# Optimization experiments

Hardware: AMD Instinct MI355X
Metric: run time of the kernel (lower is better)

Reference implementation:

```python
import jax, jax.numpy as jnp
import numpy as np

T, C_IN, H, W = 128, 3, 64, 64
HC = (32, 64)
K = 3


def _conv(x, w, b):
    # x: [1, Cin, H, W], w: [Cout, Cin, K, K] -> SAME padding
    y = jax.lax.conv_general_dilated(
        x, w, window_strides=(1, 1), padding='SAME',
        dimension_numbers=('NCHW', 'OIHW', 'NCHW'))
    return y + b[None, :, None, None]


def _run_layer(xs, w, b, hc):
    # xs: [T, Cin, H, W]; scan the ConvLSTM cell over time (batch = 1)
    h0 = jnp.zeros((1, hc, xs.shape[-2], xs.shape[-1]), xs.dtype)
    c0 = jnp.zeros_like(h0)

    def step(carry, x):
        h, c = carry
        z = _conv(jnp.concatenate([x[None], h], axis=1), w, b)  # [1, 4*hc, H, W]
        i, f, o, g = jnp.split(z, 4, axis=1)
        c_next = jax.nn.sigmoid(f) * c + jax.nn.sigmoid(i) * jnp.tanh(g)
        h_next = jax.nn.sigmoid(o) * jnp.tanh(c_next)
        return (h_next, c_next), h_next[0]

    (h, c), ys = jax.lax.scan(step, (h0, c0), xs)
    return ys, h, c  # ys: [T, hc, H, W]


def setup_inputs() -> dict:
    key = jax.random.key(0)
    ks = jax.random.split(key, 4)
    inp = {
        'input': jax.random.normal(ks[0], (T, C_IN, H, W), jnp.float32),
        'w1': jax.random.normal(ks[1], (4 * HC[0], C_IN + HC[0], K, K), jnp.float32) * 0.05,
        'b1': jnp.zeros((4 * HC[0],), jnp.float32),
        'w2': jax.random.normal(ks[2], (4 * HC[1], HC[0] + HC[1], K, K), jnp.float32) * 0.05,
        'b2': jnp.zeros((4 * HC[1],), jnp.float32),
        'fc_w': jax.random.uniform(ks[3], (6, H * W * HC[1]), jnp.float32, -0.1, 0.1),
        'fc_b': jnp.zeros((6,), jnp.float32),
    }
    return inp


def reference(input, w1, b1, w2, b2, fc_w, fc_b):
    ys1, h1, c1 = _run_layer(input, w1, b1, HC[0])
    ys2, h2, c2 = _run_layer(ys1, w2, b2, HC[1])
    outputs = ys2.reshape(ys2.shape[0], -1)          # [T, hc2*H*W]
    pose_sequence = outputs @ fc_w.T + fc_b          # [T, 6]
    return pose_sequence, h1, c1, h2, c2
```

## Files before the change

### kernel.cpp

```cpp
#include <hip/hip_runtime.h>

typedef _Float16 f16;
typedef _Float16 f16x8 __attribute__((ext_vector_type(8)));
typedef float f32x4 __attribute__((ext_vector_type(4)));
typedef unsigned short ushort_t;
typedef unsigned long long u64_t;


#define IN1SZ 209088
#define IN2ASZ 139392
#define IN2BSZ 278784
#define WP1OFF 1254528
#define WP1SZ 73728
#define WP2OFF (WP1OFF + WP1SZ)
#define WP2SZ 221184
#define FCWPOFF (WP2OFF + WP2SZ)

__device__ __forceinline__ float sigm(float x) {
  return __builtin_amdgcn_rcpf(1.0f + __expf(-x));
}
__device__ __forceinline__ float tanh_fast(float x) {
  float xc = fminf(fmaxf(x, -10.f), 10.f);
  float e = __expf(2.f * xc);
  return (e - 1.f) * __builtin_amdgcn_rcpf(e + 1.f);
}
__device__ __forceinline__ ushort_t f2u(f16 v) { return __builtin_bit_cast(ushort_t, v); }
__device__ __forceinline__ f16x8 u2f(uint4 v) { return __builtin_bit_cast(f16x8, v); }

__global__ __launch_bounds__(256) void pack_kernel(const float* __restrict__ w1,
                                                   const float* __restrict__ w2,
                                                   const float* __restrict__ fcb,
                                                   const float* __restrict__ x0,
                                                   const float* __restrict__ fcw,
                                                   float* __restrict__ pose,
                                                   ushort_t* __restrict__ wp1,
                                                   ushort_t* __restrict__ wp2,
                                                   ushort_t* __restrict__ in1hi0,
                                                   float* __restrict__ fcwp) {
  int i = blockIdx.x * 256 + threadIdx.x;
  if (i < 27648) {
    int lane = i & 63;
    int f = i >> 6;
    int mt = f & 7;
    int sm = f >> 3;
    int s = sm % 27, mb = sm / 27;
    int m = mt * 16 + (lane & 15);
    int rg = mb * 128 + m;
    int h = rg >> 2, G = rg & 3;
    int orow = G * 64 + h;
    int tap = s / 3, cb = (s % 3) * 32;
    int cq = cb + (lane >> 4) * 8;
    for (int j = 0; j < 8; ++j) {
      float v = w2[(orow * 96 + cq + j) * 9 + tap];
      wp2[f * 512 + lane * 8 + j] = f2u((f16)v);
    }
    return;
  }
  i -= 27648;
  if (i < 9216) {
    int lane = i & 63;
    int f = i >> 6;
    int mt = f & 3;
    int sm = f >> 2;
    int s = sm % 18, mb = sm / 18;
    int m = mt * 16 + (lane & 15);
    int rg = mb * 64 + m;
    int h = rg >> 2, G = rg & 3;
    int orow = G * 32 + h;
    int tap = s >> 1, cb = (s & 1) * 32;
    int cq = cb + (lane >> 4) * 8;
    for (int j = 0; j < 8; ++j) {
      int c = cq + j;
      float v = 0.f;
      if (c < 32) v = w1[(orow * 35 + c + 3) * 9 + tap];
      else if (c < 35) v = w1[(orow * 35 + c - 32) * 9 + tap];
      wp1[f * 512 + lane * 8 + j] = f2u((f16)v);
    }
    return;
  }
  i -= 9216;
  if (i < 768) { pose[i] = fcb[i % 6]; return; }
  i -= 768;
  if (i < 12288) {
    int c = i >> 12, pix = i & 4095;
    int y = pix >> 6, x = pix & 63;
    int pidx = ((y + 1) * 66 + (x + 1)) * 48 + 32 + c;
    in1hi0[pidx] = f2u((f16)x0[i]);
    return;
  }
  i -= 12288;
  if (i < 262144) {
    float* dst = fcwp + (size_t)i * 6;
#pragma unroll
    for (int j = 0; j < 6; ++j) dst[j] = fcw[(size_t)j * 262144 + i];
  }
}

template <int LAYER>
__device__ __forceinline__ void conv_body(
    int bid,
    const ushort_t* __restrict__ bhi, const ushort_t* __restrict__ b2hi,
    const ushort_t* __restrict__ wp, const float* __restrict__ bias,
    float* __restrict__ cst, float* __restrict__ hout,
    ushort_t* __restrict__ d1hi,
    ushort_t* __restrict__ d2hi,
    const float* __restrict__ fcwp, float* __restrict__ pose_t,
    const float* __restrict__ xn,
    ushort_t* Bh, ushort_t* hs, float (*red)[6]) {
  constexpr int CS = (LAYER == 1) ? 72 : 104;
  constexpr int NC32 = (LAYER == 1) ? 2 : 3;
  constexpr int NS = 9 * NC32;
  constexpr int MT = (LAYER == 1) ? 4 : 8;
  constexpr int MTPW = (LAYER == 1) ? 1 : 2;
  constexpr int H = (LAYER == 1) ? 32 : 64;
  constexpr int DEPTH = 8;
  constexpr int PRE = DEPTH - 1;

  const int tid = threadIdx.x;
  const int lane = tid & 63;
  const int w = tid >> 6;
  const int mb = bid & 1;
  const int ntile = bid >> 1;
  const int Y0 = (ntile >> 3) * 4;
  const int X0 = (ntile & 7) * 8;

  if (LAYER == 2) {
    for (int i = tid; i < 720; i += 256) {
      int hy = i / 120, rem = i % 120;
      int hx = rem / 12, c8 = rem % 12;
      int pos = (Y0 + hy) * 66 + X0 + hx;
      int dst = (hy * 10 + hx) * CS + c8 * 8;
      if (c8 < 4) {
        *(uint4*)(&Bh[dst]) = *(const uint4*)(&bhi[pos * 32 + c8 * 8]);
      } else {
        *(uint4*)(&Bh[dst]) = *(const uint4*)(&b2hi[pos * 64 + (c8 - 4) * 8]);
      }
    }
  } else {
    for (int i = tid; i < 360; i += 256) {
      int hy = i / 60, rem = i % 60;
      int hx = rem / 6, c8 = (rem % 6) * 8;
      int src = ((Y0 + hy) * 66 + X0 + hx) * 48 + c8;
      int dst = (hy * 10 + hx) * CS + c8;
      *(uint4*)(&Bh[dst]) = *(const uint4*)(&bhi[src]);
    }
    for (int i = tid; i < 120; i += 256) {
      int hp = i >> 1;
      int dst = hp * CS + 48 + (i & 1) * 8;
      *(uint4*)(&Bh[dst]) = uint4{0, 0, 0, 0};
    }
  }

  const ushort_t* aptr[MTPW];
#pragma unroll
  for (int m = 0; m < MTPW; ++m) {
    int f = (mb * NS) * MT + (w * MTPW + m);
    aptr[m] = wp + f * 512 + lane * 8;
  }
  uint4 A[DEPTH][MTPW];
  auto loada = [&](int s) {
#pragma unroll
    for (int m = 0; m < MTPW; ++m) {
      A[s % DEPTH][m] = *(const uint4*)(aptr[m] + (size_t)s * (MT * 512));
    }
  };
#pragma unroll
  for (int s = 0; s < PRE; ++s) loada(s);
  __syncthreads();

  const int n = lane & 15;
  const int q = lane >> 4;
  const int py = n >> 3, px = n & 7;

  f32x4 acc[MTPW][2];
#pragma unroll
  for (int m = 0; m < MTPW; ++m)
#pragma unroll
    for (int nt = 0; nt < 2; ++nt) acc[m][nt] = f32x4{0.f, 0.f, 0.f, 0.f};

#pragma unroll
  for (int s = 0; s < NS; ++s) {
    if (s + PRE < NS) loada(s + PRE);
    const int tap = s / NC32, cc = s % NC32;
    const int ty = tap / 3, tx = tap % 3;
    const int coff = cc * 32 + q * 8;
    f16x8 bfh[2];
#pragma unroll
    for (int nt = 0; nt < 2; ++nt) {
      int hp = (py + nt * 2 + ty) * 10 + (px + tx);
      bfh[nt] = u2f(*(const uint4*)(&Bh[hp * CS + coff]));
    }
#pragma unroll
    for (int m = 0; m < MTPW; ++m) {
      f16x8 ah = u2f(A[s % DEPTH][m]);
#pragma unroll
      for (int nt = 0; nt < 2; ++nt) {
        acc[m][nt] = __builtin_amdgcn_mfma_f32_16x16x32_f16(ah, bfh[nt], acc[m][nt], 0, 0, 0);
      }
    }
  }

  float p6[6] = {0, 0, 0, 0, 0, 0};
#pragma unroll
  for (int m = 0; m < MTPW; ++m) {
    const int ch = (w * MTPW + m) * 4 + q;
    const int hg = mb * (MT * 4) + ch;
    const float bi = bias[0 * H + hg];
    const float bf = bias[1 * H + hg];
    const float bo = bias[2 * H + hg];
    const float bg = bias[3 * H + hg];
#pragma unroll
    for (int nt = 0; nt < 2; ++nt) {
      const int pI = nt * 16 + n;
      float zi = acc[m][nt][0] + bi;
      float zf = acc[m][nt][1] + bf;
      float zo = acc[m][nt][2] + bo;
      float zg = acc[m][nt][3] + bg;
      int y = Y0 + (pI >> 3), x = X0 + (pI & 7);
      int cidx = hg * 4096 + y * 64 + x;
      float cold = cst[cidx];
      float cn = sigm(zf) * cold + sigm(zi) * tanh_fast(zg);
      float hn = sigm(zo) * tanh_fast(cn);
      cst[cidx] = cn;
      hout[cidx] = hn;
      hs[pI * 36 + ch] = f2u((f16)hn);
      if (LAYER == 2) {
#pragma unroll
        for (int j = 0; j < 6; ++j) p6[j] += hn * fcwp[(size_t)cidx * 6 + j];
      }
    }
  }
  __syncthreads();

  if (LAYER == 2) {
    int pxi = tid & 31, g = tid >> 5;
    int y = Y0 + (pxi >> 3), x = X0 + (pxi & 7);
    int pidx = (y + 1) * 66 + (x + 1);
    u64_t v = *(const u64_t*)&hs[pxi * 36 + g * 4];
    *(u64_t*)&d1hi[pidx * 64 + mb * 32 + g * 4] = v;
  } else {
    int t2 = tid & 127;
    int pxi = t2 & 31, g = t2 >> 5;
    int y = Y0 + (pxi >> 3), x = X0 + (pxi & 7);
    int pidx = (y + 1) * 66 + (x + 1);
    u64_t v = *(const u64_t*)&hs[pxi * 36 + g * 4];
    if (tid < 128) {
      *(u64_t*)&d2hi[pidx * 32 + mb * 16 + g * 4] = v;
    } else {
      *(u64_t*)&d1hi[pidx * 48 + mb * 16 + g * 4] = v;
    }
    if (mb == 0 && tid < 32) {
      int yy = Y0 + (tid >> 3), xx = X0 + (tid & 7);
      int pidx2 = (yy + 1) * 66 + (xx + 1);
#pragma unroll
      for (int c = 0; c < 3; ++c) {
        d1hi[pidx2 * 48 + 32 + c] = f2u((f16)xn[c * 4096 + yy * 64 + xx]);
      }
    }
  }

  if (LAYER == 2) {
#pragma unroll
    for (int j = 0; j < 6; ++j)
#pragma unroll
      for (int off = 32; off > 0; off >>= 1) p6[j] += __shfl_xor(p6[j], off, 64);
    if (lane == 0)
#pragma unroll
      for (int j = 0; j < 6; ++j) red[w][j] = p6[j];
    __syncthreads();
    if (tid < 6) atomicAdd(pose_t + tid, red[0][tid] + red[1][tid] + red[2][tid] + red[3][tid]);
  }
}

__global__ __launch_bounds__(256, 2) void fused_step(
    int t,
    const ushort_t* __restrict__ i1rhi, ushort_t* __restrict__ i1whi,
    const ushort_t* __restrict__ i2arhi, const ushort_t* __restrict__ i2brhi,
    ushort_t* __restrict__ i2awhi, ushort_t* __restrict__ i2bwhi,
    const ushort_t* __restrict__ wp1, const ushort_t* __restrict__ wp2,
    const float* __restrict__ b1, const float* __restrict__ b2,
    float* __restrict__ c1o, float* __restrict__ h1o,
    float* __restrict__ c2o, float* __restrict__ h2o,
    const float* __restrict__ fcwp, float* __restrict__ pose_t,
    const float* __restrict__ xn) {
  __shared__ __align__(16) ushort_t Bh[6240];
  __shared__ __align__(8) ushort_t hs[1152];
  __shared__ float red[4][6];

  int bid = blockIdx.x;
  if (bid < 256) {
    if (t >= 128) return;
    conv_body<1>(bid, i1rhi, nullptr, wp1, b1, c1o, h1o,
                 i1whi,
                 i2awhi,
                 nullptr, nullptr, xn, Bh, hs, red);
  } else {
    if (t < 1) return;
    conv_body<2>(bid - 256, i2arhi, i2brhi, wp2, b2, c2o, h2o,
                 i2bwhi,
                 nullptr,
                 fcwp, pose_t, nullptr, Bh, hs, red);
  }
}

extern "C" void kernel_launch(void* const* d_in, const int* in_sizes, int n_in, void* d_out,
                              int out_size, void* d_ws, size_t ws_size, hipStream_t stream) {
  const float* input = (const float*)d_in[0];
  const float* w1 = (const float*)d_in[1];
  const float* b1 = (const float*)d_in[2];
  const float* w2 = (const float*)d_in[3];
  const float* b2 = (const float*)d_in[4];
  const float* fcw = (const float*)d_in[5];
  const float* fcb = (const float*)d_in[6];

  float* out = (float*)d_out;
  float* pose = out;
  float* h1o = out + 768;
  float* c1o = h1o + 131072;
  float* h2o = c1o + 131072;
  float* c2o = h2o + 262144;

  ushort_t* ws = (ushort_t*)d_ws;
  ushort_t* in1hi[2] = {ws, ws + IN1SZ};
  ushort_t* ab = ws + 2 * IN1SZ;
  ushort_t* i2ahi[2] = {ab, ab + IN2ASZ};
  ushort_t* bb = ab + 2 * IN2ASZ;
  ushort_t* i2bhi[2] = {bb, bb + IN2BSZ};
  ushort_t* wp1 = ws + WP1OFF;
  ushort_t* wp2 = ws + WP2OFF;
  float* fcwp = (float*)(ws + FCWPOFF);

  hipMemsetAsync(ws, 0, (size_t)WP1OFF * 2, stream);
  hipMemsetAsync(c1o, 0, (size_t)655360 * 4, stream);
  pack_kernel<<<1219, 256, 0, stream>>>(w1, w2, fcb, input, fcw, pose, wp1, wp2,
                                        in1hi[0], fcwp);

  for (int t = 0; t <= 128; ++t) {
    int p = t & 1, pn = p ^ 1;
    int tn = (t + 1 < 128) ? t + 1 : 127;
    float* pose_t = pose + ((t > 0) ? (t - 1) * 6 : 0);
    fused_step<<<512, 256, 0, stream>>>(
        t,
        in1hi[p], in1hi[pn],
        i2ahi[pn], i2bhi[pn],
        i2ahi[p], i2bhi[p],
        wp1, wp2, b1, b2, c1o, h1o, c2o, h2o,
        fcwp, pose_t,
        input + (size_t)tn * 12288);
  }
}
```

Baseline: 1.565 ms.

## Fuse two timesteps per launch using a software grid barrier

Each launch now runs two consecutive ConvLSTM timesteps, so the kernel count drops from 129 to 65. Inside a launch the steps are separated by a flag-based grid barrier: every block publishes a flag and block 0 gathers them and releases a generation counter. This is meant to remove per-launch overhead and the drain/refill gap between steps. It depends on all 512 blocks being co-resident and adds spin-wait and fence latency at each in-kernel barrier.

```diff
diff --git a/kernel.cpp b/kernel.cpp
--- a/kernel.cpp
+++ b/kernel.cpp
@@ -10,11 +10,13 @@
 #define IN1SZ 209088
 #define IN2ASZ 139392
 #define IN2BSZ 278784
-#define WP1OFF 1254528
+#define BAROFF 1254528
+#define WP1OFF 1258624
 #define WP1SZ 73728
 #define WP2OFF (WP1OFF + WP1SZ)
 #define WP2SZ 221184
 #define FCWPOFF (WP2OFF + WP2SZ)
+#define NBLOCKS 512
 
 __device__ __forceinline__ float sigm(float x) {
   return __builtin_amdgcn_rcpf(1.0f + __expf(-x));
@@ -26,6 +28,31 @@
 }
 __device__ __forceinline__ ushort_t f2u(f16 v) { return __builtin_bit_cast(ushort_t, v); }
 __device__ __forceinline__ f16x8 u2f(uint4 v) { return __builtin_bit_cast(f16x8, v); }
+
+__device__ __forceinline__ void grid_barrier(int* flags, int* gen, int it) {
+  __syncthreads();
+  if (threadIdx.x == 0) {
+    __builtin_amdgcn_fence(__ATOMIC_RELEASE, "agent");
+    __hip_atomic_store(&flags[blockIdx.x], it, __ATOMIC_RELAXED,
+                       __HIP_MEMORY_SCOPE_AGENT);
+  }
+  if (blockIdx.x == 0) {
+    const int i0 = threadIdx.x, i1 = threadIdx.x + 256;
+    for (;;) {
+      int a = __hip_atomic_load(&flags[i0], __ATOMIC_RELAXED, __HIP_MEMORY_SCOPE_AGENT);
+      int b = __hip_atomic_load(&flags[i1], __ATOMIC_RELAXED, __HIP_MEMORY_SCOPE_AGENT);
+      if (__syncthreads_and(a >= it && b >= it)) break;
+      __builtin_amdgcn_s_sleep(1);
+    }
+    if (threadIdx.x == 0)
+      __hip_atomic_store(gen, it, __ATOMIC_RELAXED, __HIP_MEMORY_SCOPE_AGENT);
+  } else if (threadIdx.x == 0) {
+    while (__hip_atomic_load(gen, __ATOMIC_RELAXED, __HIP_MEMORY_SCOPE_AGENT) < it)
+      __builtin_amdgcn_s_sleep(1);
+  }
+  __syncthreads();
+  asm volatile("" ::: "memory");
+}
 
 __global__ __launch_bounds__(256) void pack_kernel(const float* __restrict__ w1,
                                                    const float* __restrict__ w2,
@@ -272,34 +299,47 @@
   }
 }
 
-__global__ __launch_bounds__(256, 2) void fused_step(
-    int t,
-    const ushort_t* __restrict__ i1rhi, ushort_t* __restrict__ i1whi,
-    const ushort_t* __restrict__ i2arhi, const ushort_t* __restrict__ i2brhi,
-    ushort_t* __restrict__ i2awhi, ushort_t* __restrict__ i2bwhi,
+__global__ __launch_bounds__(256, 2) void fused_pair(
+    int t0, int nsteps,
+    ushort_t* __restrict__ in1_0, ushort_t* __restrict__ in1_1,
+    ushort_t* __restrict__ i2a_0, ushort_t* __restrict__ i2a_1,
+    ushort_t* __restrict__ i2b_0, ushort_t* __restrict__ i2b_1,
     const ushort_t* __restrict__ wp1, const ushort_t* __restrict__ wp2,
     const float* __restrict__ b1, const float* __restrict__ b2,
     float* __restrict__ c1o, float* __restrict__ h1o,
     float* __restrict__ c2o, float* __restrict__ h2o,
-    const float* __restrict__ fcwp, float* __restrict__ pose_t,
-    const float* __restrict__ xn) {
+    const float* __restrict__ fcwp, float* __restrict__ pose,
+    const float* __restrict__ input, int* __restrict__ bar) {
   __shared__ __align__(16) ushort_t Bh[6240];
   __shared__ __align__(8) ushort_t hs[1152];
   __shared__ float red[4][6];
 
-  int bid = blockIdx.x;
-  if (bid < 256) {
-    if (t >= 128) return;
-    conv_body<1>(bid, i1rhi, nullptr, wp1, b1, c1o, h1o,
-                 i1whi,
-                 i2awhi,
-                 nullptr, nullptr, xn, Bh, hs, red);
-  } else {
-    if (t < 1) return;
-    conv_body<2>(bid - 256, i2arhi, i2brhi, wp2, b2, c2o, h2o,
-                 i2bwhi,
-                 nullptr,
-                 fcwp, pose_t, nullptr, Bh, hs, red);
+  const int bid = blockIdx.x;
+  ushort_t* in1[2] = {in1_0, in1_1};
+  ushort_t* i2a[2] = {i2a_0, i2a_1};
+  ushort_t* i2b[2] = {i2b_0, i2b_1};
+
+  for (int k = 0; k < nsteps; ++k) {
+    const int t = t0 + k;
+    const int p = t & 1, pn = p ^ 1;
+    if (bid < 256) {
+      if (t < 128) {
+        int tn = (t + 1 < 128) ? t + 1 : 127;
+        conv_body<1>(bid, in1[p], nullptr, wp1, b1, c1o, h1o,
+                     in1[pn],
+                     i2a[p],
+                     nullptr, nullptr,
+                     input + (size_t)tn * 12288, Bh, hs, red);
+      }
+    } else {
+      if (t >= 1) {
+        conv_body<2>(bid - 256, i2a[pn], i2b[pn], wp2, b2, c2o, h2o,
+                     i2b[p],
+                     nullptr,
+                     fcwp, pose + (t - 1) * 6, nullptr, Bh, hs, red);
+      }
+    }
+    if (k + 1 < nsteps) grid_barrier(bar, bar + 544, t + 1);
   }
 }
 
@@ -321,11 +361,15 @@
   float* c2o = h2o + 262144;
 
   ushort_t* ws = (ushort_t*)d_ws;
-  ushort_t* in1hi[2] = {ws, ws + IN1SZ};
+  ushort_t* in1_0 = ws;
+  ushort_t* in1_1 = ws + IN1SZ;
   ushort_t* ab = ws + 2 * IN1SZ;
-  ushort_t* i2ahi[2] = {ab, ab + IN2ASZ};
+  ushort_t* i2a_0 = ab;
+  ushort_t* i2a_1 = ab + IN2ASZ;
   ushort_t* bb = ab + 2 * IN2ASZ;
-  ushort_t* i2bhi[2] = {bb, bb + IN2BSZ};
+  ushort_t* i2b_0 = bb;
+  ushort_t* i2b_1 = bb + IN2BSZ;
+  int* bar = (int*)(ws + BAROFF);
   ushort_t* wp1 = ws + WP1OFF;
   ushort_t* wp2 = ws + WP2OFF;
   float* fcwp = (float*)(ws + FCWPOFF);
@@ -333,19 +377,14 @@
   hipMemsetAsync(ws, 0, (size_t)WP1OFF * 2, stream);
   hipMemsetAsync(c1o, 0, (size_t)655360 * 4, stream);
   pack_kernel<<<1219, 256, 0, stream>>>(w1, w2, fcb, input, fcw, pose, wp1, wp2,
-                                        in1hi[0], fcwp);
-
-  for (int t = 0; t <= 128; ++t) {
-    int p = t & 1, pn = p ^ 1;
-    int tn = (t + 1 < 128) ? t + 1 : 127;
-    float* pose_t = pose + ((t > 0) ? (t - 1) * 6 : 0);
-    fused_step<<<512, 256, 0, stream>>>(
-        t,
-        in1hi[p], in1hi[pn],
-        i2ahi[pn], i2bhi[pn],
-        i2ahi[p], i2bhi[p],
+                                        in1_0, fcwp);
+
+  for (int t0 = 0; t0 <= 128; t0 += 2) {
+    int nsteps = (t0 < 128) ? 2 : 1;
+    fused_pair<<<NBLOCKS, 256, 0, stream>>>(
+        t0, nsteps,
+        in1_0, in1_1, i2a_0, i2a_1, i2b_0, i2b_1,
         wp1, wp2, b1, b2, c1o, h1o, c2o, h2o,
-        fcwp, pose_t,
-        input + (size_t)tn * 12288);
-  }
-}
+        fcwp, pose, input, bar);
+  }
+}
```

After: 3.440 ms. +119.8%, slower.

## Share layer-1 hidden buffer with layer 2 and hoist state/FC loads

Applied to the files above, without the earlier changes.

Layer 2 now reads h1 directly from layer 1's padded input buffer (channel stride 48) instead of a separate 32-channel copy. This removes one half-precision store per pixel per step and shrinks the workspace. The cell-state and FC-weight loads are also issued before the MFMA loop, so their latency overlaps with the convolution. The cost is more live registers during the main loop, which may pressure occupancy at launch bounds (256, 2).

```diff
diff --git a/kernel.cpp b/kernel.cpp
--- a/kernel.cpp
+++ b/kernel.cpp
@@ -8,9 +8,8 @@
 
 
 #define IN1SZ 209088
-#define IN2ASZ 139392
 #define IN2BSZ 278784
-#define WP1OFF 1254528
+#define WP1OFF 975744
 #define WP1SZ 73728
 #define WP2OFF (WP1OFF + WP1SZ)
 #define WP2SZ 221184
@@ -103,7 +102,6 @@
     const ushort_t* __restrict__ wp, const float* __restrict__ bias,
     float* __restrict__ cst, float* __restrict__ hout,
     ushort_t* __restrict__ d1hi,
-    ushort_t* __restrict__ d2hi,
     const float* __restrict__ fcwp, float* __restrict__ pose_t,
     const float* __restrict__ xn,
     ushort_t* Bh, ushort_t* hs, float (*red)[6]) {
@@ -131,7 +129,7 @@
       int pos = (Y0 + hy) * 66 + X0 + hx;
       int dst = (hy * 10 + hx) * CS + c8 * 8;
       if (c8 < 4) {
-        *(uint4*)(&Bh[dst]) = *(const uint4*)(&bhi[pos * 32 + c8 * 8]);
+        *(uint4*)(&Bh[dst]) = *(const uint4*)(&bhi[pos * 48 + c8 * 8]);
       } else {
         *(uint4*)(&Bh[dst]) = *(const uint4*)(&b2hi[pos * 64 + (c8 - 4) * 8]);
       }
@@ -151,6 +149,29 @@
     }
   }
 
+  const int n = lane & 15;
+  const int q = lane >> 4;
+  int cidxs[MTPW][2];
+  float cold[MTPW][2];
+  float fw[MTPW][2][6];
+#pragma unroll
+  for (int m = 0; m < MTPW; ++m) {
+    const int ch = (w * MTPW + m) * 4 + q;
+    const int hg = mb * (MT * 4) + ch;
+#pragma unroll
+    for (int nt = 0; nt < 2; ++nt) {
+      const int pI = nt * 16 + n;
+      int y = Y0 + (pI >> 3), x = X0 + (pI & 7);
+      int cidx = hg * 4096 + y * 64 + x;
+      cidxs[m][nt] = cidx;
+      cold[m][nt] = cst[cidx];
+      if (LAYER == 2) {
+#pragma unroll
+        for (int j = 0; j < 6; ++j) fw[m][nt][j] = fcwp[(size_t)cidx * 6 + j];
+      }
+    }
+  }
+
   const ushort_t* aptr[MTPW];
 #pragma unroll
   for (int m = 0; m < MTPW; ++m) {
@@ -168,8 +189,6 @@
   for (int s = 0; s < PRE; ++s) loada(s);
   __syncthreads();
 
-  const int n = lane & 15;
-  const int q = lane >> 4;
   const int py = n >> 3, px = n & 7;
 
   f32x4 acc[MTPW][2];
@@ -216,17 +235,15 @@
       float zf = acc[m][nt][1] + bf;
       float zo = acc[m][nt][2] + bo;
       float zg = acc[m][nt][3] + bg;
-      int y = Y0 + (pI >> 3), x = X0 + (pI & 7);
-      int cidx = hg * 4096 + y * 64 + x;
-      float cold = cst[cidx];
-      float cn = sigm(zf) * cold + sigm(zi) * tanh_fast(zg);
+      int cidx = cidxs[m][nt];
+      float cn = sigm(zf) * cold[m][nt] + sigm(zi) * tanh_fast(zg);
       float hn = sigm(zo) * tanh_fast(cn);
       cst[cidx] = cn;
       hout[cidx] = hn;
       hs[pI * 36 + ch] = f2u((f16)hn);
       if (LAYER == 2) {
 #pragma unroll
-        for (int j = 0; j < 6; ++j) p6[j] += hn * fcwp[(size_t)cidx * 6 + j];
+        for (int j = 0; j < 6; ++j) p6[j] += hn * fw[m][nt][j];
       }
     }
   }
@@ -239,18 +256,16 @@
     u64_t v = *(const u64_t*)&hs[pxi * 36 + g * 4];
     *(u64_t*)&d1hi[pidx * 64 + mb * 32 + g * 4] = v;
   } else {
-    int t2 = tid & 127;
-    int pxi = t2 & 31, g = t2 >> 5;
-    int y = Y0 + (pxi >> 3), x = X0 + (pxi & 7);
-    int pidx = (y + 1) * 66 + (x + 1);
-    u64_t v = *(const u64_t*)&hs[pxi * 36 + g * 4];
     if (tid < 128) {
-      *(u64_t*)&d2hi[pidx * 32 + mb * 16 + g * 4] = v;
-    } else {
+      int pxi = tid & 31, g = tid >> 5;
+      int y = Y0 + (pxi >> 3), x = X0 + (pxi & 7);
+      int pidx = (y + 1) * 66 + (x + 1);
+      u64_t v = *(const u64_t*)&hs[pxi * 36 + g * 4];
       *(u64_t*)&d1hi[pidx * 48 + mb * 16 + g * 4] = v;
     }
-    if (mb == 0 && tid < 32) {
-      int yy = Y0 + (tid >> 3), xx = X0 + (tid & 7);
+    if (mb == 0 && tid >= 128 && tid < 160) {
+      int t2 = tid - 128;
+      int yy = Y0 + (t2 >> 3), xx = X0 + (t2 & 7);
       int pidx2 = (yy + 1) * 66 + (xx + 1);
 #pragma unroll
       for (int c = 0; c < 3; ++c) {
@@ -275,8 +290,7 @@
 __global__ __launch_bounds__(256, 2) void fused_step(
     int t,
     const ushort_t* __restrict__ i1rhi, ushort_t* __restrict__ i1whi,
-    const ushort_t* __restrict__ i2arhi, const ushort_t* __restrict__ i2brhi,
-    ushort_t* __restrict__ i2awhi, ushort_t* __restrict__ i2bwhi,
+    const ushort_t* __restrict__ i2brhi, ushort_t* __restrict__ i2bwhi,
     const ushort_t* __restrict__ wp1, const ushort_t* __restrict__ wp2,
     const float* __restrict__ b1, const float* __restrict__ b2,
     float* __restrict__ c1o, float* __restrict__ h1o,
@@ -292,13 +306,11 @@
     if (t >= 128) return;
     conv_body<1>(bid, i1rhi, nullptr, wp1, b1, c1o, h1o,
                  i1whi,
-                 i2awhi,
                  nullptr, nullptr, xn, Bh, hs, red);
   } else {
     if (t < 1) return;
-    conv_body<2>(bid - 256, i2arhi, i2brhi, wp2, b2, c2o, h2o,
+    conv_body<2>(bid - 256, i1rhi, i2brhi, wp2, b2, c2o, h2o,
                  i2bwhi,
-                 nullptr,
                  fcwp, pose_t, nullptr, Bh, hs, red);
   }
 }
@@ -322,9 +334,7 @@
 
   ushort_t* ws = (ushort_t*)d_ws;
   ushort_t* in1hi[2] = {ws, ws + IN1SZ};
-  ushort_t* ab = ws + 2 * IN1SZ;
-  ushort_t* i2ahi[2] = {ab, ab + IN2ASZ};
-  ushort_t* bb = ab + 2 * IN2ASZ;
+  ushort_t* bb = ws + 2 * IN1SZ;
   ushort_t* i2bhi[2] = {bb, bb + IN2BSZ};
   ushort_t* wp1 = ws + WP1OFF;
   ushort_t* wp2 = ws + WP2OFF;
@@ -342,8 +352,7 @@
     fused_step<<<512, 256, 0, stream>>>(
         t,
         in1hi[p], in1hi[pn],
-        i2ahi[pn], i2bhi[pn],
-        i2ahi[p], i2bhi[p],
+        i2bhi[pn], i2bhi[p],
         wp1, wp2, b1, b2, c1o, h1o, c2o, h2o,
         fcwp, pose_t,
         input + (size_t)tn * 12288);
```

Result: slower. 1.669 ms (+6.6%).
